# Kernel optimization log

Hardware: AMD Instinct MI355X
Metric: run time of the kernel (lower is better)

## Reference

```python
import jax, jax.numpy as jnp
import numpy as np

DIM = 1024
NUM_HEADS = 16
HEAD_DIM = DIM // NUM_HEADS
SCALE = HEAD_DIM ** -0.5


def setup_inputs() -> dict:
    key = jax.random.key(0)
    k_x, k_qw, k_qb, k_pw, k_pb = jax.random.split(key, 5)
    B, N = 4, 4096
    x = jax.random.normal(k_x, (B, N, DIM), dtype=jnp.float32)
    # nn.Linear(dim, 3*dim): weight (out, in), bias (out,)
    s = DIM ** -0.5
    qkv_w = jax.random.uniform(k_qw, (3 * DIM, DIM), jnp.float32, -s, s)
    qkv_b = jax.random.uniform(k_qb, (3 * DIM,), jnp.float32, -s, s)
    proj_w = jax.random.uniform(k_pw, (DIM, DIM), jnp.float32, -s, s)
    proj_b = jax.random.uniform(k_pb, (DIM,), jnp.float32, -s, s)
    return {"x": x, "qkv_w": qkv_w, "qkv_b": qkv_b,
            "proj_w": proj_w, "proj_b": proj_b}


def reference(x, qkv_w, qkv_b, proj_w, proj_b):
    B, N, C = x.shape
    H, D = NUM_HEADS, HEAD_DIM
    # qkv projection: (B,N,3C) -> (B,N,3,H,D)
    qkv = (jnp.einsum('bnc,oc->bno', x, qkv_w) + qkv_b).reshape(B, N, 3, H, D)
    q, k, v = qkv[:, :, 0], qkv[:, :, 1], qkv[:, :, 2]  # each (B,N,H,D)
    # Faithful to source: matmul over the last two dims of (B,N,H,D),
    # i.e. attention scores over the HEAD axis per token -> (B,N,H,H).
    attn = jnp.einsum('bnhd,bngd->bnhg', q, k) * SCALE
    attn = jax.nn.softmax(attn, axis=-1)
    out = jnp.einsum('bnhg,bngd->bnhd', attn, v)      # (B,N,H,D)
    # torch: .transpose(1,2).reshape(B,N,C) -> (B,H,N,D) reshaped to (B,N,C)
    out = out.transpose(0, 2, 1, 3).reshape(B, N, C)
    return jnp.einsum('bnc,oc->bno', out, proj_w) + proj_b
```

## Files before the change

### kernel.cpp

```cpp
#include <hip/hip_runtime.h>
#include <hip/hip_bf16.h>

#define TOK   16384
#define KD    1024
#define NQKV  3072
#define SEQL  4096
#define ATT_SCALE 0.125f

typedef __attribute__((ext_vector_type(4))) float f32x4;
typedef __attribute__((ext_vector_type(8))) short bf16x8;

__device__ __forceinline__ unsigned short f2b(float f){
    union { float f; unsigned u; } x; x.f = f;
    return (unsigned short)((x.u + 0x7FFFu + ((x.u >> 16) & 1u)) >> 16);
}
__device__ __forceinline__ float b2f(unsigned short s){
    union { unsigned u; float f; } x; x.u = ((unsigned)s) << 16;
    return x.f;
}
__device__ __forceinline__ bf16x8 lds8(const unsigned short* p){
    union { uint4 u; bf16x8 v; } t; t.u = *(const uint4*)p; return t.v;
}
__device__ __forceinline__ void glds16(const void* g, void* l){
    __builtin_amdgcn_global_load_lds((const __attribute__((address_space(1))) unsigned*)g,
                                     (__attribute__((address_space(3))) unsigned*)l, 16, 0, 0);
}

__global__ __launch_bounds__(256) void cvt_kernel(const float* __restrict__ in,
                                                  unsigned short* __restrict__ out, int n)
{
    int i = (blockIdx.x * 256 + threadIdx.x) * 8;
    if (i >= n) return;
    float4 a = *(const float4*)(in + i);
    float4 b = *(const float4*)(in + i + 4);
    union { unsigned short u[8]; uint4 v; } t;
    t.u[0]=f2b(a.x); t.u[1]=f2b(a.y); t.u[2]=f2b(a.z); t.u[3]=f2b(a.w);
    t.u[4]=f2b(b.x); t.u[5]=f2b(b.y); t.u[6]=f2b(b.z); t.u[7]=f2b(b.w);
    *(uint4*)(out + i) = t.v;
}

template<bool OUT_BF16>
__global__ __launch_bounds__(512, 2) void gemm256(const unsigned short* __restrict__ A,
        const unsigned short* __restrict__ Bw, const float* __restrict__ bias,
        void* __restrict__ Cp, int Nn)
{
    extern __shared__ unsigned short sm[];
    unsigned short* As = sm;
    unsigned short* Bs = sm + 32768;

    const int tid = threadIdx.x, lane = tid & 63;
    const int w = tid >> 6, wm = w >> 2, wn = w & 3;
    const int rl = lane & 15, kslot = lane >> 4;

    const int gx = gridDim.x;
    const int nwg = gx * gridDim.y;
    int id = blockIdx.y * gx + blockIdx.x;
    id = (id & 7) * (nwg >> 3) + (id >> 3);
    const int cBase = (id % gx) * 256;
    const int mBase = (id / gx) * 256;

    const int srow = tid >> 2;
    const int sseg = ((tid & 3) ^ ((tid >> 2) & 3)) * 8;
    const unsigned short* Ag = A  + (size_t)(mBase + srow) * KD + sseg;
    const unsigned short* Bg = Bw + (size_t)(cBase + srow) * KD + sseg;

    const int psg = (kslot ^ (rl & 3)) * 8;
    const int aoff = (wm * 128 + rl) * 32 + psg;
    const int boff = (wn * 64  + rl) * 32 + psg;

    f32x4 acc[8][4];
    #pragma unroll
    for (int m = 0; m < 8; m++)
        #pragma unroll
        for (int n = 0; n < 4; n++) acc[m][n] = (f32x4)0.f;

#define STAGE(bb, kk) { \
        glds16(Ag + (kk),            As + (bb)*8192 + tid*8); \
        glds16(Ag + 128*KD + (kk),   As + (bb)*8192 + 4096 + tid*8); \
        glds16(Bg + (kk),            Bs + (bb)*8192 + tid*8); \
        glds16(Bg + 128*KD + (kk),   Bs + (bb)*8192 + 4096 + tid*8); }

#define DSREAD(bb) { \
        const unsigned short* a_ = As + (bb)*8192; \
        const unsigned short* b_ = Bs + (bb)*8192; \
        _Pragma("unroll") \
        for (int m = 0; m < 8; m++) af[m] = lds8(a_ + aoff + m * 512); \
        _Pragma("unroll") \
        for (int n = 0; n < 4; n++) bf[n] = lds8(b_ + boff + n * 512); }

#define MFMA32() { \
        __builtin_amdgcn_s_setprio(1); \
        _Pragma("unroll") \
        for (int m = 0; m < 8; m++) \
            _Pragma("unroll") \
            for (int n = 0; n < 4; n++) \
                acc[m][n] = __builtin_amdgcn_mfma_f32_16x16x32_bf16(af[m], bf[n], acc[m][n], 0, 0, 0); \
        __builtin_amdgcn_s_setprio(0); }

    bf16x8 af[8], bf[4];

    STAGE(0, 0)
    STAGE(1, 32)

    for (int t = 0; t < 30; ++t) {
        STAGE((t + 2) & 3, (t + 2) * 32)
        asm volatile("s_waitcnt vmcnt(8)" ::: "memory");
        __builtin_amdgcn_s_barrier();
        DSREAD(t & 3)
        __builtin_amdgcn_s_barrier();
        asm volatile("s_waitcnt lgkmcnt(0)" ::: "memory");
        __builtin_amdgcn_sched_barrier(0);
        MFMA32()
    }
    asm volatile("s_waitcnt vmcnt(4)" ::: "memory");
    __builtin_amdgcn_s_barrier();
    DSREAD(2)
    __builtin_amdgcn_s_barrier();
    asm volatile("s_waitcnt lgkmcnt(0)" ::: "memory");
    __builtin_amdgcn_sched_barrier(0);
    MFMA32()
    asm volatile("s_waitcnt vmcnt(0)" ::: "memory");
    __builtin_amdgcn_s_barrier();
    DSREAD(3)
    asm volatile("s_waitcnt lgkmcnt(0)" ::: "memory");
    __builtin_amdgcn_sched_barrier(0);
    MFMA32()
#undef STAGE
#undef DSREAD
#undef MFMA32

    float bv[4];
    #pragma unroll
    for (int n = 0; n < 4; n++) bv[n] = bias[cBase + wn * 64 + n * 16 + rl];
    #pragma unroll
    for (int m = 0; m < 8; m++) {
        #pragma unroll
        for (int i = 0; i < 4; i++) {
            const size_t row = mBase + wm * 128 + m * 16 + kslot * 4 + i;
            #pragma unroll
            for (int n = 0; n < 4; n++) {
                const int col = cBase + wn * 64 + n * 16 + rl;
                const float val = acc[m][n][i] + bv[n];
                if (OUT_BF16) ((unsigned short*)Cp)[row * Nn + col] = f2b(val);
                else          ((float*)Cp)[row * Nn + col] = val;
            }
        }
    }
}

__global__ __launch_bounds__(256) void attn_kernel(const unsigned short* __restrict__ qkv,
                                                   unsigned short* __restrict__ outp)
{
    __shared__ __align__(16) unsigned short qs[4][48 * 72];
    __shared__ float ps[4][16 * 17];
    const int tid = threadIdx.x, w = tid >> 6, lane = tid & 63;
    const int t = blockIdx.x * 4 + w;

    const unsigned short* src = qkv + (size_t)t * NQKV;
    #pragma unroll
    for (int i = 0; i < 6; i++) {
        const int e = i * 512 + lane * 8;
        uint4 v = *(const uint4*)(src + e);
        *(uint4*)&qs[w][(e >> 6) * 72 + (e & 63)] = v;
    }
    __syncthreads();

    const int h = lane & 15, g0 = lane >> 4;
    uint4 qv[8];
    #pragma unroll
    for (int i = 0; i < 8; i++) qv[i] = *(const uint4*)&qs[w][h * 72 + i * 8];
    float s[4];
    #pragma unroll
    for (int i = 0; i < 4; i++) {
        const int g = g0 * 4 + i;
        float a = 0.f;
        #pragma unroll
        for (int c = 0; c < 8; c++) {
            uint4 kv = *(const uint4*)&qs[w][(16 + g) * 72 + c * 8];
            uint qa[4] = {qv[c].x, qv[c].y, qv[c].z, qv[c].w};
            uint ka[4] = {kv.x, kv.y, kv.z, kv.w};
            #pragma unroll
            for (int u = 0; u < 4; u++) {
                a += b2f((unsigned short)qa[u]) * b2f((unsigned short)ka[u]);
                a += b2f((unsigned short)(qa[u] >> 16)) * b2f((unsigned short)(ka[u] >> 16));
            }
        }
        s[i] = a * ATT_SCALE;
    }
    float mx = fmaxf(fmaxf(s[0], s[1]), fmaxf(s[2], s[3]));
    mx = fmaxf(mx, __shfl_xor(mx, 16, 64));
    mx = fmaxf(mx, __shfl_xor(mx, 32, 64));
    float p[4], smv = 0.f;
    #pragma unroll
    for (int i = 0; i < 4; i++) { p[i] = __expf(s[i] - mx); smv += p[i]; }
    smv += __shfl_xor(smv, 16, 64);
    smv += __shfl_xor(smv, 32, 64);
    const float inv = 1.f / smv;
    #pragma unroll
    for (int i = 0; i < 4; i++) ps[w][h * 17 + g0 * 4 + i] = p[i] * inv;
    __syncthreads();

    const int h2 = lane >> 2, db = (lane & 3) * 16;
    float pr[16];
    #pragma unroll
    for (int g = 0; g < 16; g++) pr[g] = ps[w][h2 * 17 + g];
    float acc[16];
    #pragma unroll
    for (int j = 0; j < 16; j++) acc[j] = 0.f;
    #pragma unroll
    for (int g = 0; g < 16; g++) {
        const unsigned short* vp = &qs[w][(32 + g) * 72 + db];
        uint4 v0 = *(const uint4*)vp;
        uint4 v1 = *(const uint4*)(vp + 8);
        const float pg = pr[g];
        uint va[8] = {v0.x, v0.y, v0.z, v0.w, v1.x, v1.y, v1.z, v1.w};
        #pragma unroll
        for (int u = 0; u < 8; u++) {
            acc[2*u]   += pg * b2f((unsigned short)va[u]);
            acc[2*u+1] += pg * b2f((unsigned short)(va[u] >> 16));
        }
    }
    const int b = t >> 12, n = t & 4095;
    const int n1 = h2 * 256 + (n >> 4);
    const int c0 = (n & 15) * 64 + db;
    union { unsigned short u[16]; uint4 v[2]; } st;
    #pragma unroll
    for (int j = 0; j < 16; j++) st.u[j] = f2b(acc[j]);
    unsigned short* dst = outp + ((size_t)(b * SEQL + n1)) * 1024 + c0;
    *(uint4*)dst       = st.v[0];
    *(uint4*)(dst + 8) = st.v[1];
}

extern "C" void kernel_launch(void* const* d_in, const int* in_sizes, int n_in,
                              void* d_out, int out_size, void* d_ws, size_t ws_size,
                              hipStream_t stream)
{
    const float* x      = (const float*)d_in[0];
    const float* qkv_w  = (const float*)d_in[1];
    const float* qkv_b  = (const float*)d_in[2];
    const float* proj_w = (const float*)d_in[3];
    const float* proj_b = (const float*)d_in[4];

    unsigned short* xb  = (unsigned short*)d_ws;
    unsigned short* qkv = xb + (size_t)TOK * KD;
    unsigned short* qwb = qkv + (size_t)TOK * NQKV;
    unsigned short* pwb = qwb + (size_t)NQKV * KD;
    unsigned short* att = xb;

    hipFuncSetAttribute(reinterpret_cast<const void*>(&gemm256<true>),
                        hipFuncAttributeMaxDynamicSharedMemorySize, 131072);
    hipFuncSetAttribute(reinterpret_cast<const void*>(&gemm256<false>),
                        hipFuncAttributeMaxDynamicSharedMemorySize, 131072);

    cvt_kernel<<<dim3(TOK * KD / 2048), dim3(256), 0, stream>>>(x, xb, TOK * KD);
    cvt_kernel<<<dim3(NQKV * KD / 2048), dim3(256), 0, stream>>>(qkv_w, qwb, NQKV * KD);
    cvt_kernel<<<dim3(KD * KD / 2048), dim3(256), 0, stream>>>(proj_w, pwb, KD * KD);

    gemm256<true><<<dim3(NQKV / 256, TOK / 256), dim3(512), 131072, stream>>>(
        xb, qwb, qkv_b, qkv, NQKV);
    attn_kernel<<<dim3(TOK / 4), dim3(256), 0, stream>>>(qkv, att);
    gemm256<false><<<dim3(KD / 256, TOK / 256), dim3(512), 131072, stream>>>(
        att, pwb, proj_b, (float*)d_out, KD);
}
```

Baseline: 228.2 us.

## Restructure GEMM mainloop to BK=64 double buffer with interleaved half-tile staging

```diff
diff --git a/kernel.cpp b/kernel.cpp
--- a/kernel.cpp
+++ b/kernel.cpp
@@ -44,9 +44,9 @@
         const unsigned short* __restrict__ Bw, const float* __restrict__ bias,
         void* __restrict__ Cp, int Nn)
 {
-    extern __shared__ unsigned short sm[];
-    unsigned short* As = sm;
-    unsigned short* Bs = sm + 32768;
+    extern __shared__ unsigned short smem[];
+    unsigned short* As = smem;
+    unsigned short* Bs = smem + 32768;
 
     const int tid = threadIdx.x, lane = tid & 63;
     const int w = tid >> 6, wm = w >> 2, wn = w & 3;
@@ -59,14 +59,15 @@
     const int cBase = (id % gx) * 256;
     const int mBase = (id / gx) * 256;
 
-    const int srow = tid >> 2;
-    const int sseg = ((tid & 3) ^ ((tid >> 2) & 3)) * 8;
-    const unsigned short* Ag = A  + (size_t)(mBase + srow) * KD + sseg;
-    const unsigned short* Bg = Bw + (size_t)(cBase + srow) * KD + sseg;
-
-    const int psg = (kslot ^ (rl & 3)) * 8;
-    const int aoff = (wm * 128 + rl) * 32 + psg;
-    const int boff = (wn * 64  + rl) * 32 + psg;
+    const int u = tid >> 3;
+    const int seg8 = ((tid & 7) ^ (u & 7)) * 8;
+    const unsigned short* Ag = A  + (size_t)(mBase + u) * KD + seg8;
+    const unsigned short* Bg = Bw + (size_t)(cBase + (u >> 4) * 64 + (u & 15)) * KD + seg8;
+
+    const int arow = (wm * 16 + rl) * 64;
+    const int brow = (wn * 16 + rl) * 64;
+    const int psg0 = (kslot ^ (rl & 7)) * 8;
+    const int psg1 = ((kslot + 4) ^ (rl & 7)) * 8;
 
     f32x4 acc[8][4];
     #pragma unroll
@@ -74,60 +75,98 @@
         #pragma unroll
         for (int n = 0; n < 4; n++) acc[m][n] = (f32x4)0.f;
 
-#define STAGE(bb, kk) { \
-        glds16(Ag + (kk),            As + (bb)*8192 + tid*8); \
-        glds16(Ag + 128*KD + (kk),   As + (bb)*8192 + 4096 + tid*8); \
-        glds16(Bg + (kk),            Bs + (bb)*8192 + tid*8); \
-        glds16(Bg + 128*KD + (kk),   Bs + (bb)*8192 + 4096 + tid*8); }
-
-#define DSREAD(bb) { \
-        const unsigned short* a_ = As + (bb)*8192; \
-        const unsigned short* b_ = Bs + (bb)*8192; \
+#define STAGE_AH0(bb, kk) { glds16(Ag + (kk),            As + (bb)*16384 + tid*8); \
+                            glds16(Ag + 64*KD + (kk),    As + (bb)*16384 + 4096  + tid*8); }
+#define STAGE_AH1(bb, kk) { glds16(Ag + 128*KD + (kk),   As + (bb)*16384 + 8192  + tid*8); \
+                            glds16(Ag + 192*KD + (kk),   As + (bb)*16384 + 12288 + tid*8); }
+#define STAGE_BH0(bb, kk) { glds16(Bg + (kk),            Bs + (bb)*16384 + tid*8); \
+                            glds16(Bg + 16*KD + (kk),    Bs + (bb)*16384 + 4096  + tid*8); }
+#define STAGE_BH1(bb, kk) { glds16(Bg + 32*KD + (kk),    Bs + (bb)*16384 + 8192  + tid*8); \
+                            glds16(Bg + 48*KD + (kk),    Bs + (bb)*16384 + 12288 + tid*8); }
+
+#define RDA(a_, half) { _Pragma("unroll") \
+    for (int m = 0; m < 4; m++) { \
+        af[m][0] = lds8((a_) + (half)*8192 + arow + m*2048 + psg0); \
+        af[m][1] = lds8((a_) + (half)*8192 + arow + m*2048 + psg1); } }
+#define RDB(b_, nlo) { _Pragma("unroll") \
+    for (int n = 0; n < 2; n++) { \
+        bf[(nlo)+n][0] = lds8((b_) + brow + ((nlo)+n)*4096 + psg0); \
+        bf[(nlo)+n][1] = lds8((b_) + brow + ((nlo)+n)*4096 + psg1); } }
+
+#define MM16(mb, nb) { \
+    __builtin_amdgcn_s_setprio(1); \
+    _Pragma("unroll") \
+    for (int m = 0; m < 4; m++) \
         _Pragma("unroll") \
-        for (int m = 0; m < 8; m++) af[m] = lds8(a_ + aoff + m * 512); \
-        _Pragma("unroll") \
-        for (int n = 0; n < 4; n++) bf[n] = lds8(b_ + boff + n * 512); }
-
-#define MFMA32() { \
-        __builtin_amdgcn_s_setprio(1); \
-        _Pragma("unroll") \
-        for (int m = 0; m < 8; m++) \
-            _Pragma("unroll") \
-            for (int n = 0; n < 4; n++) \
-                acc[m][n] = __builtin_amdgcn_mfma_f32_16x16x32_bf16(af[m], bf[n], acc[m][n], 0, 0, 0); \
-        __builtin_amdgcn_s_setprio(0); }
-
-    bf16x8 af[8], bf[4];
-
-    STAGE(0, 0)
-    STAGE(1, 32)
-
-    for (int t = 0; t < 30; ++t) {
-        STAGE((t + 2) & 3, (t + 2) * 32)
-        asm volatile("s_waitcnt vmcnt(8)" ::: "memory");
-        __builtin_amdgcn_s_barrier();
-        DSREAD(t & 3)
-        __builtin_amdgcn_s_barrier();
-        asm volatile("s_waitcnt lgkmcnt(0)" ::: "memory");
-        __builtin_amdgcn_sched_barrier(0);
-        MFMA32()
-    }
-    asm volatile("s_waitcnt vmcnt(4)" ::: "memory");
-    __builtin_amdgcn_s_barrier();
-    DSREAD(2)
-    __builtin_amdgcn_s_barrier();
-    asm volatile("s_waitcnt lgkmcnt(0)" ::: "memory");
-    __builtin_amdgcn_sched_barrier(0);
-    MFMA32()
-    asm volatile("s_waitcnt vmcnt(0)" ::: "memory");
-    __builtin_amdgcn_s_barrier();
-    DSREAD(3)
-    asm volatile("s_waitcnt lgkmcnt(0)" ::: "memory");
-    __builtin_amdgcn_sched_barrier(0);
-    MFMA32()
-#undef STAGE
-#undef DSREAD
-#undef MFMA32
+        for (int n = 0; n < 2; n++) { \
+            acc[(mb)+m][(nb)+n] = __builtin_amdgcn_mfma_f32_16x16x32_bf16(af[m][0], bf[(nb)+n][0], acc[(mb)+m][(nb)+n], 0, 0, 0); \
+            acc[(mb)+m][(nb)+n] = __builtin_amdgcn_mfma_f32_16x16x32_bf16(af[m][1], bf[(nb)+n][1], acc[(mb)+m][(nb)+n], 0, 0, 0); } \
+    __builtin_amdgcn_s_setprio(0); }
+
+#define WAITLGKM { asm volatile("s_waitcnt lgkmcnt(0)" ::: "memory"); __builtin_amdgcn_sched_barrier(0); }
+
+    bf16x8 af[4][2], bf[4][2];
+
+    STAGE_AH0(0, 0)
+    STAGE_BH0(0, 0)
+    STAGE_BH1(0, 0)
+    STAGE_AH1(0, 0)
+
+    int buf = 0;
+    for (int t = 0; t < 15; ++t) {
+        const unsigned short* a = As + buf * 16384;
+        const unsigned short* b = Bs + buf * 16384;
+        const int nk = (t + 1) * 64;
+        STAGE_AH0(buf ^ 1, nk)
+        asm volatile("s_waitcnt vmcnt(6)" ::: "memory");
+        __builtin_amdgcn_s_barrier();
+        RDA(a, 0) RDB(b, 0)
+        WAITLGKM
+        MM16(0, 0)
+        STAGE_BH0(buf ^ 1, nk)
+        asm volatile("s_waitcnt vmcnt(6)" ::: "memory");
+        __builtin_amdgcn_s_barrier();
+        RDB(b, 2)
+        WAITLGKM
+        MM16(0, 2)
+        STAGE_BH1(buf ^ 1, nk)
+        asm volatile("s_waitcnt vmcnt(6)" ::: "memory");
+        __builtin_amdgcn_s_barrier();
+        RDA(a, 1)
+        WAITLGKM
+        MM16(4, 0)
+        STAGE_AH1(buf ^ 1, nk)
+        MM16(4, 2)
+        buf ^= 1;
+    }
+    {
+        const unsigned short* a = As + buf * 16384;
+        const unsigned short* b = Bs + buf * 16384;
+        asm volatile("s_waitcnt vmcnt(4)" ::: "memory");
+        __builtin_amdgcn_s_barrier();
+        RDA(a, 0) RDB(b, 0)
+        WAITLGKM
+        MM16(0, 0)
+        asm volatile("s_waitcnt vmcnt(2)" ::: "memory");
+        __builtin_amdgcn_s_barrier();
+        RDB(b, 2)
+        WAITLGKM
+        MM16(0, 2)
+        asm volatile("s_waitcnt vmcnt(0)" ::: "memory");
+        __builtin_amdgcn_s_barrier();
+        RDA(a, 1)
+        WAITLGKM
+        MM16(4, 0)
+        MM16(4, 2)
+    }
+#undef STAGE_AH0
+#undef STAGE_AH1
+#undef STAGE_BH0
+#undef STAGE_BH1
+#undef RDA
+#undef RDB
+#undef MM16
+#undef WAITLGKM
 
     float bv[4];
     #pragma unroll
@@ -136,7 +175,7 @@
     for (int m = 0; m < 8; m++) {
         #pragma unroll
         for (int i = 0; i < 4; i++) {
-            const size_t row = mBase + wm * 128 + m * 16 + kslot * 4 + i;
+            const size_t row = mBase + (m >> 2) * 128 + (m & 3) * 32 + wm * 16 + kslot * 4 + i;
             #pragma unroll
             for (int n = 0; n < 4; n++) {
                 const int col = cBase + wn * 64 + n * 16 + rl;
@@ -180,9 +219,9 @@
             uint qa[4] = {qv[c].x, qv[c].y, qv[c].z, qv[c].w};
             uint ka[4] = {kv.x, kv.y, kv.z, kv.w};
             #pragma unroll
-            for (int u = 0; u < 4; u++) {
-                a += b2f((unsigned short)qa[u]) * b2f((unsigned short)ka[u]);
-                a += b2f((unsigned short)(qa[u] >> 16)) * b2f((unsigned short)(ka[u] >> 16));
+            for (int uu = 0; uu < 4; uu++) {
+                a += b2f((unsigned short)qa[uu]) * b2f((unsigned short)ka[uu]);
+                a += b2f((unsigned short)(qa[uu] >> 16)) * b2f((unsigned short)(ka[uu] >> 16));
             }
         }
         s[i] = a * ATT_SCALE;
@@ -215,9 +254,9 @@
         const float pg = pr[g];
         uint va[8] = {v0.x, v0.y, v0.z, v0.w, v1.x, v1.y, v1.z, v1.w};
         #pragma unroll
-        for (int u = 0; u < 8; u++) {
-            acc[2*u]   += pg * b2f((unsigned short)va[u]);
-            acc[2*u+1] += pg * b2f((unsigned short)(va[u] >> 16));
+        for (int uu = 0; uu < 8; uu++) {
+            acc[2*uu]   += pg * b2f((unsigned short)va[uu]);
+            acc[2*uu+1] += pg * b2f((unsigned short)(va[uu] >> 16));
         }
     }
     const int b = t >> 12, n = t & 4095;
```

Measured after the change: 201.1 us. 1.13x faster.
